# Performance work log

Measured on AMD Instinct MI355X. Metric: run time of the kernel, lower is better.

## Reference

```python
import jax, jax.numpy as jnp
import numpy as np

C = 64; NET = 32; K = 3; G = 4; GC = C // G; P = K * K
STRIDE = 1; PAD = 1; DIL = 1; OFFSET_SCALE = 1.0
BN_EPS = 1e-5; LN_EPS = 1e-6


def conv2d(x, w, b, groups=1, pad=1):
    # x: (N,C,H,W), w: (O, I//groups, kh, kw)
    y = jax.lax.conv_general_dilated(
        x, w, (1, 1), [(pad, pad), (pad, pad)],
        feature_group_count=groups,
        dimension_numbers=('NCHW', 'OIHW', 'NCHW'))
    return y + b[None, :, None, None]


def dcnv3_core(x, offset, mask):
    """Faithful port of dcnv3_core_pytorch (InternImage).
    x: (N,H,W,C) channels-last; offset: (N,H,W,G*P*2); mask: (N,H,W,G*P) (softmaxed).
    grid_sample(bilinear, zeros padding, align_corners=False) done manually."""
    xp = jnp.pad(x, ((0, 0), (PAD, PAD), (PAD, PAD), (0, 0)))
    N, Hin, Win, _ = xp.shape
    Ho, Wo = offset.shape[1], offset.shape[2]
    # reference points in normalized [0,1] coords (x first, y second)
    start = (DIL * (K - 1)) // 2 + 0.5
    ref_x = (start + jnp.arange(Wo, dtype=jnp.float32) * STRIDE) / Win  # (Wo,)
    ref_y = (start + jnp.arange(Ho, dtype=jnp.float32) * STRIDE) / Hin  # (Ho,)
    ref = jnp.stack(jnp.broadcast_arrays(ref_x[None, :], ref_y[:, None]), axis=-1)  # (Ho,Wo,2)
    # dilation grid (kernel tap offsets, torch meshgrid 'ij' flatten order: w-major)
    kv = (jnp.arange(K, dtype=jnp.float32) * DIL - (DIL * (K - 1)) // 2)
    gx, gy = jnp.meshgrid(kv / Win, kv / Hin, indexing='ij')
    grid = jnp.stack([gx, gy], -1).reshape(P, 2)  # (P,2), same for every group
    # sampling locations, normalized: (N,Ho,Wo,G,P,2)
    off = offset.reshape(N, Ho, Wo, G, P, 2) * (OFFSET_SCALE / jnp.array([Win, Hin], jnp.float32))
    loc = ref[None, :, :, None, None, :] + grid[None, None, None, None, :, :] * OFFSET_SCALE + off
    # grid_sample align_corners=False: pixel = loc*size - 0.5  (since g = 2*loc-1)
    px = loc[..., 0] * Win - 0.5
    py = loc[..., 1] * Hin - 0.5
    x0 = jnp.floor(px); y0 = jnp.floor(py)
    ix0 = x0.astype(jnp.int32); iy0 = y0.astype(jnp.int32)
    wx1 = px - x0; wy1 = py - y0; wx0 = 1.0 - wx1; wy0 = 1.0 - wy1
    xg = xp.reshape(N, Hin, Win, G, GC)
    n_idx = jnp.arange(N)[:, None, None, None, None]
    g_idx = jnp.arange(G)[None, None, None, :, None]

    def sample(ix, iy):
        valid = ((ix >= 0) & (ix < Win) & (iy >= 0) & (iy < Hin)).astype(xg.dtype)
        v = xg[n_idx, jnp.clip(iy, 0, Hin - 1), jnp.clip(ix, 0, Win - 1), g_idx]  # (N,Ho,Wo,G,P,GC)
        return v * valid[..., None]

    val = (sample(ix0, iy0) * (wx0 * wy0)[..., None]
           + sample(ix0 + 1, iy0) * (wx1 * wy0)[..., None]
           + sample(ix0, iy0 + 1) * (wx0 * wy1)[..., None]
           + sample(ix0 + 1, iy0 + 1) * (wx1 * wy1)[..., None])
    out = jnp.einsum('nhwgpc,nhwgp->nhwgc', val, mask.reshape(N, Ho, Wo, G, P))
    return out.reshape(N, Ho, Wo, C)


def setup_inputs() -> dict:
    key = jax.random.key(0)
    ks = jax.random.split(key, 16)
    N, H, W = 4, 128, 128
    f = lambda k, shp, s=1.0: jax.random.normal(k, shp, jnp.float32) * s
    return {
        'input_x': f(ks[0], (N, C, H, W)),
        'input_y': f(ks[1], (N, NET, H, W)),
        'enc_w': f(ks[2], (NET, C), 0.05), 'enc_b': jnp.zeros((NET,), jnp.float32),
        'bn_g': jnp.ones((NET,), jnp.float32), 'bn_b': jnp.zeros((NET,), jnp.float32),
        'bn_m': jnp.zeros((NET,), jnp.float32), 'bn_v': jnp.ones((NET,), jnp.float32),
        'gru_wz': f(ks[3], (NET, 2 * NET, 3, 3), 0.05), 'gru_bz': jnp.zeros((NET,), jnp.float32),
        'gru_wr': f(ks[4], (NET, 2 * NET, 3, 3), 0.05), 'gru_br': jnp.zeros((NET,), jnp.float32),
        'gru_wq': f(ks[5], (NET, 2 * NET, 3, 3), 0.05), 'gru_bq': jnp.zeros((NET,), jnp.float32),
        'dw_w': f(ks[6], (C, 1, 3, 3), 0.1), 'dw_b': jnp.zeros((C,), jnp.float32),
        'ln_g': jnp.ones((C,), jnp.float32), 'ln_b': jnp.zeros((C,), jnp.float32),
        'off_w': f(ks[7], (G * P * 2, C), 0.1), 'off_b': f(ks[8], (G * P * 2,), 0.1),
        'mask_w': f(ks[9], (G * P, C), 0.1), 'mask_b': jnp.zeros((G * P,), jnp.float32),
        'inp_w': f(ks[10], (C, C), 0.1), 'inp_b': jnp.zeros((C,), jnp.float32),
        'out_w': f(ks[11], (C, C), 0.1), 'out_b': jnp.zeros((C,), jnp.float32),
    }


def reference(input_x, input_y, enc_w, enc_b, bn_g, bn_b, bn_m, bn_v,
              gru_wz, gru_bz, gru_wr, gru_br, gru_wq, gru_bq,
              dw_w, dw_b, ln_g, ln_b, off_w, off_b, mask_w, mask_b,
              inp_w, inp_b, out_w, out_b):
    N, _, H, W = input_x.shape
    # encoder: 1x1 Conv + BN(eval) + SiLU
    e = jnp.einsum('nchw,oc->nohw', input_x, enc_w) + enc_b[None, :, None, None]
    e = (e - bn_m[None, :, None, None]) * jax.lax.rsqrt(bn_v + BN_EPS)[None, :, None, None]
    e = e * bn_g[None, :, None, None] + bn_b[None, :, None, None]
    x_en = jax.nn.silu(e)
    # ConvGRU: h' = (1-z)*h + z*q
    hx = jnp.concatenate([input_y, x_en], axis=1)
    z = jax.nn.sigmoid(conv2d(hx, gru_wz, gru_bz))
    r = jax.nn.sigmoid(conv2d(hx, gru_wr, gru_br))
    q = jnp.tanh(conv2d(jnp.concatenate([r * input_y, x_en], axis=1), gru_wq, gru_bq))
    h = (1.0 - z) * input_y + z * q  # (N,NET,H,W)
    # channels-last main path
    inp = input_x.transpose(0, 2, 3, 1)  # (N,H,W,C)
    x = inp @ inp_w.T + inp_b
    # depthwise conv on gru state -> LN (channels_last) -> GELU
    y = conv2d(h, dw_w, dw_b, groups=NET).transpose(0, 2, 3, 1)  # (N,H,W,C)
    mu = y.mean(-1, keepdims=True)
    var = ((y - mu) ** 2).mean(-1, keepdims=True)
    y = (y - mu) * jax.lax.rsqrt(var + LN_EPS) * ln_g + ln_b
    y = jax.nn.gelu(y, approximate=False)
    offset = y @ off_w.T + off_b  # (N,H,W,G*P*2)
    m = y @ mask_w.T + mask_b
    m = jax.nn.softmax(m.reshape(N, H, W, G, P), axis=-1).reshape(N, H, W, G * P)
    x = dcnv3_core(x, offset, m)
    x = x @ out_w.T + out_b
    return jax.nn.silu(x.transpose(0, 3, 1, 2)), h
```

## Files before the change

kernel.cpp:

```cpp
#include <hip/hip_runtime.h>
#include <hip/hip_bf16.h>

typedef __hip_bfloat16 bf16;
typedef short short8v __attribute__((ext_vector_type(8)));
typedef short short4v __attribute__((ext_vector_type(4)));
typedef float float4v __attribute__((ext_vector_type(4)));

static __device__ __forceinline__ float b2f(bf16 v){ return __bfloat162float(v); }
static __device__ __forceinline__ bf16 f2b(float v){ return __float2bfloat16(v); }
static __device__ __forceinline__ float bu2f(unsigned short u){ return __uint_as_float(((unsigned)u) << 16); }
static __device__ __forceinline__ short f2bs(float v){ bf16 t = __float2bfloat16(v); return *(short*)&t; }

#define WT 128
#define HWT 16384

#define OFF_ENC   0
#define OFF_ENCSC 2048
#define OFF_ENCSH 2080
#define OFF_BZ    20544
#define OFF_BR    39008
#define OFF_BQ    57472
#define OFF_DWP   57504
#define OFF_DWB   58080
#define OFF_LNG   58144
#define OFF_LNB   58208
#define OFF_OMB   65184
#define OFF_WINP  65296
#define OFF_BINP  69392
#define OFF_BOUT  73552
#define NW_TOTAL  73616
#define NBF_ZR    36864
#define NBF_Q     18432
#define NBF_OM    7168
#define NBF_OUT   4096
#define NPREP     (NW_TOTAL + NBF_ZR + NBF_Q + NBF_OM + NBF_OUT)
#define NHALO     2064
#define NTOT      (NPREP + NHALO)

#define B_WZRB  294912
#define B_WQB   368640
#define B_WOMB  405504
#define B_WOUTB 419840
#define B_HXP   428544
#define B_QINP  9081344
#define B_ZBUF  17734144
#define B_XL    428544

__global__ void k_prep(
    const float* __restrict__ enc_w, const float* __restrict__ enc_b,
    const float* __restrict__ bn_g, const float* __restrict__ bn_b,
    const float* __restrict__ bn_m, const float* __restrict__ bn_v,
    const float* __restrict__ gwz, const float* __restrict__ gbz,
    const float* __restrict__ gwr, const float* __restrict__ gbr,
    const float* __restrict__ gwq, const float* __restrict__ gbq,
    const float* __restrict__ dww, const float* __restrict__ dwb,
    const float* __restrict__ lng, const float* __restrict__ lnb,
    const float* __restrict__ offw, const float* __restrict__ offb,
    const float* __restrict__ maskw, const float* __restrict__ maskb,
    const float* __restrict__ inpw, const float* __restrict__ inpb,
    const float* __restrict__ outw, const float* __restrict__ outb,
    float* __restrict__ Wp, bf16* __restrict__ wzrb, bf16* __restrict__ wqb,
    bf16* __restrict__ womb, bf16* __restrict__ woutb,
    bf16* __restrict__ hxp, bf16* __restrict__ qinp) {
  int i = blockIdx.x * blockDim.x + threadIdx.x;
  if (i >= NTOT) return;
  if (i >= NPREP) {
    int t = i - NPREP;
    int img = t / 516, r = t % 516;
    int ph, pw;
    if (r < 130) { ph = 0; pw = r; }
    else if (r < 260) { ph = 129; pw = r - 130; }
    else if (r < 388) { ph = r - 260 + 1; pw = 0; }
    else { ph = r - 388 + 1; pw = 129; }
    size_t pb = (((size_t)img * 130 + ph) * 130 + pw) * 64;
    uint4 zz = make_uint4(0, 0, 0, 0);
    #pragma unroll
    for (int k = 0; k < 8; ++k) {
      ((uint4*)(hxp + pb))[k] = zz;
      ((uint4*)(qinp + pb))[k] = zz;
    }
    return;
  }
  if (i >= NW_TOTAL) {
    int d = i - NW_TOTAL;
    if (d < NBF_ZR) {
      int t = d / 9216, rem = d % 9216;
      int kc = rem / 512, rem2 = rem % 512;
      int ln = rem2 >> 3, j = rem2 & 7;
      int n = t * 16 + (ln & 15);
      int cin = (kc & 1) * 32 + ((ln >> 4) << 3) + j;
      int tap = kc >> 1;
      float v = (n < 32) ? gwz[(n*64 + cin)*9 + tap] : gwr[((n-32)*64 + cin)*9 + tap];
      wzrb[d] = f2b(v);
    } else if (d < NBF_ZR + NBF_Q) {
      int d2 = d - NBF_ZR;
      int t = d2 / 9216, rem = d2 % 9216;
      int kc = rem / 512, rem2 = rem % 512;
      int ln = rem2 >> 3, j = rem2 & 7;
      int n = t * 16 + (ln & 15);
      int cin = (kc & 1) * 32 + ((ln >> 4) << 3) + j;
      int tap = kc >> 1;
      wqb[d2] = f2b(gwq[(n*64 + cin)*9 + tap]);
    } else if (d < NBF_ZR + NBF_Q + NBF_OM) {
      int d3 = d - NBF_ZR - NBF_Q;
      int wv = d3 / 1024, rem = d3 % 1024;
      int kc = rem / 512, rem2 = rem % 512;
      int ln = rem2 >> 3, j = rem2 & 7;
      int jcol = wv * 16 + (ln & 15);
      int c = kc * 32 + ((ln >> 4) << 3) + j;
      float v = (jcol < 72) ? offw[jcol*64 + c] : ((jcol < 108) ? maskw[(jcol-72)*64 + c] : 0.f);
      womb[d3] = f2b(v);
    } else {
      int d4 = d - NBF_ZR - NBF_Q - NBF_OM;
      int wv = d4 / 1024, rem = d4 % 1024;
      int kc = rem / 512, rem2 = rem % 512;
      int ln = rem2 >> 3, j = rem2 & 7;
      int o = wv * 16 + (ln & 15);
      int c = kc * 32 + ((ln >> 4) << 3) + j;
      woutb[d4] = f2b(outw[o*64 + c]);
    }
    return;
  }
  float v;
  if (i < 2048) { int c = i >> 5, o = i & 31; v = enc_w[o*64 + c]; }
  else if (i < 2080) { int o = i - 2048; v = bn_g[o] * rsqrtf(bn_v[o] + 1e-5f); }
  else if (i < 2112) { int o = i - 2080;
    float sc = bn_g[o] * rsqrtf(bn_v[o] + 1e-5f);
    v = (enc_b[o] - bn_m[o]) * sc + bn_b[o]; }
  else if (i < 20544) { v = 0.f; }
  else if (i < 20576) { v = gbz[i - OFF_BZ]; }
  else if (i < 39008) { v = 0.f; }
  else if (i < 39040) { v = gbr[i - OFF_BR]; }
  else if (i < 57472) { v = 0.f; }
  else if (i < 57504) { v = gbq[i - OFF_BQ]; }
  else if (i < 58080) { int d = i - OFF_DWP; int tap = d >> 6, o = d & 63; v = dww[o*9 + tap]; }
  else if (i < 58144) { v = dwb[i - OFF_DWB]; }
  else if (i < 58208) { v = lng[i - OFF_LNG]; }
  else if (i < 58272) { v = lnb[i - OFF_LNB]; }
  else if (i < 65184) { v = 0.f; }
  else if (i < 65292) { int j = i - OFF_OMB; v = (j < 72) ? offb[j] : maskb[j-72]; }
  else if (i < 65296) { v = 0.f; }
  else if (i < 69392) { int d = i - OFF_WINP; int c = d >> 6, o = d & 63; v = inpw[o*64 + c]; }
  else if (i < 69456) { v = inpb[i - OFF_BINP]; }
  else if (i < 73552) { v = 0.f; }
  else { v = outb[i - OFF_BOUT]; }
  Wp[i] = v;
}

__global__ void __launch_bounds__(256) k_pre(
    const float* __restrict__ X, const float* __restrict__ Y,
    const float* __restrict__ Wp, bf16* __restrict__ hxp, bf16* __restrict__ qinp) {
  __shared__ float xls[4096];
  int tid = threadIdx.x;
  int px = tid & 63, sect = tid >> 6;
  int img = blockIdx.z, h = blockIdx.y, w0 = blockIdx.x * 64;
  int hw = h * WT + w0 + px;
  const float* xp = X + (size_t)img * (64 * HWT) + hw;
  #pragma unroll
  for (int i = 0; i < 16; ++i) {
    int c = sect * 16 + i;
    xls[c * 64 + px] = xp[c * HWT];
  }
  const float* yp = Y + (size_t)img * (32 * HWT) + hw;
  bf16 yv[8];
  #pragma unroll
  for (int i = 0; i < 8; ++i) yv[i] = f2b(yp[(sect * 8 + i) * HWT]);
  size_t pb = (((size_t)img * 130 + h + 1) * 130 + (w0 + px + 1)) * 64;
  *(uint4*)(hxp + pb + sect * 8) = *(const uint4*)yv;
  __syncthreads();
  float aen[8];
  #pragma unroll
  for (int o = 0; o < 8; ++o) aen[o] = 0.f;
  for (int k = 0; k < 64; ++k) {
    float a = xls[k * 64 + px];
    const float* we = Wp + OFF_ENC + k * 32 + sect * 8;
    #pragma unroll
    for (int o = 0; o < 8; ++o) aen[o] += a * we[o];
  }
  bf16 xe[8];
  #pragma unroll
  for (int o = 0; o < 8; ++o) {
    int oo = sect * 8 + o;
    float e = aen[o] * Wp[OFF_ENCSC + oo] + Wp[OFF_ENCSH + oo];
    xe[o] = f2b(e / (1.f + __expf(-e)));
  }
  *(uint4*)(hxp + pb + 32 + sect * 8) = *(const uint4*)xe;
  *(uint4*)(qinp + pb + 32 + sect * 8) = *(const uint4*)xe;
}

__global__ void __launch_bounds__(256) k_zr(
    const float* __restrict__ Wp,
    const bf16* __restrict__ hxp, const bf16* __restrict__ wzrb,
    bf16* __restrict__ qinp, bf16* __restrict__ zbuf) {
  __shared__ short zt[32 * 132];
  __shared__ short ryt[128 * 40];
  int tid = threadIdx.x;
  int wv = tid >> 6, ln = tid & 63;
  int quad = ln >> 4, lm = ln & 15;
  int img = blockIdx.z, h = blockIdx.y;
  int p0 = wv * 32;
  const short* hs = (const short*)hxp;
  const short* ws = (const short*)wzrb;
  size_t rowb = ((size_t)img * 130 + h + 1) * 130;
  const short* ab0 = hs + (rowb + p0 + lm + 1) * 64 + quad * 8;
  const short* ab1 = ab0 + 16 * 64;
  short8v a0[18], a1[18];
  #pragma unroll
  for (int kc = 0; kc < 18; ++kc) {
    const int tap = kc >> 1, cin0 = (kc & 1) * 32;
    const int dd = (tap / 3 - 1) * 130 + (tap % 3 - 1);
    a0[kc] = *(const short8v*)(ab0 + dd * 64 + cin0);
    a1[kc] = *(const short8v*)(ab1 + dd * 64 + cin0);
  }
  float4v acc[8];
  #pragma unroll
  for (int t = 0; t < 8; ++t) acc[t] = (float4v){0.f, 0.f, 0.f, 0.f};
  #pragma unroll
  for (int kc = 0; kc < 18; ++kc) {
    #pragma unroll
    for (int t = 0; t < 4; ++t) {
      short8v b = *(const short8v*)(ws + ((t * 18 + kc) * 64 + ln) * 8);
      acc[t*2]   = __builtin_amdgcn_mfma_f32_16x16x32_bf16(a0[kc], b, acc[t*2], 0, 0, 0);
      acc[t*2+1] = __builtin_amdgcn_mfma_f32_16x16x32_bf16(a1[kc], b, acc[t*2+1], 0, 0, 0);
    }
  }
  #pragma unroll
  for (int mt = 0; mt < 2; ++mt) {
    #pragma unroll
    for (int t = 0; t < 2; ++t) {
      int n = t * 16 + lm;
      float bz = Wp[OFF_BZ + n];
      short zp[4];
      #pragma unroll
      for (int ri = 0; ri < 4; ++ri)
        zp[ri] = f2bs(1.f / (1.f + __expf(-(acc[t*2+mt][ri] + bz))));
      *(short4v*)(zt + n * 132 + p0 + mt * 16 + quad * 4) = *(const short4v*)zp;
    }
  }
  #pragma unroll
  for (int mt = 0; mt < 2; ++mt) {
    #pragma unroll
    for (int t = 2; t < 4; ++t) {
      int c = (t - 2) * 16 + lm;
      float br = Wp[OFF_BR + c];
      #pragma unroll
      for (int ri = 0; ri < 4; ++ri) {
        int px = p0 + mt * 16 + quad * 4 + ri;
        float rv = 1.f / (1.f + __expf(-(acc[t*2+mt][ri] + br)));
        float yy = b2f(hxp[(rowb + px + 1) * 64 + c]);
        ryt[px * 40 + c] = f2bs(rv * yy);
      }
    }
  }
  __syncthreads();
  {
    int n2 = tid >> 3, pq = tid & 7;
    short8v z0 = *(const short8v*)(zt + n2 * 132 + pq * 16);
    short8v z1 = *(const short8v*)(zt + n2 * 132 + pq * 16 + 8);
    short* zo = (short*)zbuf + (((size_t)img * 128 + h) * 32 + n2) * 128 + pq * 16;
    *(short8v*)zo = z0;
    *(short8v*)(zo + 8) = z1;
  }
  {
    int px = tid >> 1, chalf = tid & 1;
    short8v r0 = *(const short8v*)(ryt + px * 40 + chalf * 16);
    short8v r1 = *(const short8v*)(ryt + px * 40 + chalf * 16 + 8);
    short* qo = (short*)qinp + (rowb + px + 1) * 64 + chalf * 16;
    *(short8v*)qo = r0;
    *(short8v*)(qo + 8) = r1;
  }
}

__global__ void __launch_bounds__(256) k_qg(
    const float* __restrict__ Y, const float* __restrict__ Wp,
    const bf16* __restrict__ qinp, const bf16* __restrict__ wqb,
    const bf16* __restrict__ zbuf, float* __restrict__ outh) {
  __shared__ float hout[32 * 132];
  int tid = threadIdx.x;
  int wv = tid >> 6, ln = tid & 63;
  int quad = ln >> 4, lm = ln & 15;
  int img = blockIdx.z, h = blockIdx.y;
  int p0 = wv * 32;
  const short* qs = (const short*)qinp;
  const short* ws = (const short*)wqb;
  size_t rowb = ((size_t)img * 130 + h + 1) * 130;
  const short* ab0 = qs + (rowb + p0 + lm + 1) * 64 + quad * 8;
  const short* ab1 = ab0 + 16 * 64;
  short8v a0[18], a1[18];
  #pragma unroll
  for (int kc = 0; kc < 18; ++kc) {
    const int tap = kc >> 1, cin0 = (kc & 1) * 32;
    const int dd = (tap / 3 - 1) * 130 + (tap % 3 - 1);
    a0[kc] = *(const short8v*)(ab0 + dd * 64 + cin0);
    a1[kc] = *(const short8v*)(ab1 + dd * 64 + cin0);
  }
  float4v acc[4];
  #pragma unroll
  for (int t = 0; t < 4; ++t) acc[t] = (float4v){0.f, 0.f, 0.f, 0.f};
  #pragma unroll
  for (int kc = 0; kc < 18; ++kc) {
    #pragma unroll
    for (int t = 0; t < 2; ++t) {
      short8v b = *(const short8v*)(ws + ((t * 18 + kc) * 64 + ln) * 8);
      acc[t*2]   = __builtin_amdgcn_mfma_f32_16x16x32_bf16(a0[kc], b, acc[t*2], 0, 0, 0);
      acc[t*2+1] = __builtin_amdgcn_mfma_f32_16x16x32_bf16(a1[kc], b, acc[t*2+1], 0, 0, 0);
    }
  }
  #pragma unroll
  for (int mt = 0; mt < 2; ++mt) {
    #pragma unroll
    for (int t = 0; t < 2; ++t) {
      int n = t * 16 + lm;
      float bq = Wp[OFF_BQ + n];
      float4 hv;
      hv.x = acc[t*2+mt][0] + bq; hv.y = acc[t*2+mt][1] + bq;
      hv.z = acc[t*2+mt][2] + bq; hv.w = acc[t*2+mt][3] + bq;
      *(float4*)(hout + n * 132 + p0 + mt * 16 + quad * 4) = hv;
    }
  }
  __syncthreads();
  const short* zbb = (const short*)zbuf + ((size_t)img * 128 + h) * 32 * 128;
  #pragma unroll
  for (int r = 0; r < 4; ++r) {
    int n = (tid >> 5) + r * 8;
    int px4 = (tid & 31) * 4;
    float4 hv = *(const float4*)(hout + n * 132 + px4);
    uint2 zz = *(const uint2*)(zbb + n * 128 + px4);
    size_t gb = ((size_t)img * 32 + n) * HWT + h * 128 + px4;
    float4 yv = *(const float4*)(Y + gb);
    float z0 = bu2f((unsigned short)(zz.x & 0xFFFFu)), z1 = bu2f((unsigned short)(zz.x >> 16));
    float z2 = bu2f((unsigned short)(zz.y & 0xFFFFu)), z3 = bu2f((unsigned short)(zz.y >> 16));
    float4 o;
    o.x = (1.f - z0) * yv.x + z0 * tanhf(hv.x);
    o.y = (1.f - z1) * yv.y + z1 * tanhf(hv.y);
    o.z = (1.f - z2) * yv.z + z2 * tanhf(hv.z);
    o.w = (1.f - z3) * yv.w + z3 * tanhf(hv.w);
    *(float4*)(outh + gb) = o;
  }
}

__global__ void __launch_bounds__(256) k_xl(
    const float* __restrict__ X, const float* __restrict__ Wp, bf16* __restrict__ xl) {
  __shared__ float xls[4096];
  int tid = threadIdx.x;
  int px = tid & 63, sect = tid >> 6;
  int img = blockIdx.z, h = blockIdx.y, w0 = blockIdx.x * 64;
  int hw = h * WT + w0 + px;
  const float* xp = X + (size_t)img * (64 * HWT) + hw;
  #pragma unroll
  for (int i = 0; i < 16; ++i) {
    int c = sect * 16 + i;
    xls[c * 64 + px] = xp[c * HWT];
  }
  __syncthreads();
  float acc[16];
  #pragma unroll
  for (int o = 0; o < 16; ++o) acc[o] = Wp[OFF_BINP + sect * 16 + o];
  for (int k = 0; k < 64; ++k) {
    float a = xls[k * 64 + px];
    const float* wr = Wp + OFF_WINP + k * 64 + sect * 16;
    #pragma unroll
    for (int o = 0; o < 16; ++o) acc[o] += a * wr[o];
  }
  bf16 ov[16];
  #pragma unroll
  for (int o = 0; o < 16; ++o) ov[o] = f2b(acc[o]);
  bf16* op = xl + ((size_t)img * HWT + hw) * 64 + sect * 16;
  ((uint4*)op)[0] = ((const uint4*)ov)[0];
  ((uint4*)op)[1] = ((const uint4*)ov)[1];
}

#define LDS_PSA  0
#define LDS_PSB  2048
#define LDS_STAT 4096
#define LDS_Y    4608
#define LDS_OM   13824
#define LDS_TOT  28416

__global__ void __launch_bounds__(512) k_mega(
    const float* __restrict__ Wp, const float* __restrict__ hb,
    const bf16* __restrict__ xl, const bf16* __restrict__ womb,
    const bf16* __restrict__ woutb, float* __restrict__ out0) {
  __shared__ char smem[LDS_TOT];
  float* psa  = (float*)(smem + LDS_PSA);
  float* psb  = (float*)(smem + LDS_PSB);
  float* stat = (float*)(smem + LDS_STAT);
  short* yls  = (short*)(smem + LDS_Y);
  short* omls = (short*)(smem + LDS_OM);
  short* vls  = (short*)(smem + LDS_Y);

  int tid = threadIdx.x;
  int img = blockIdx.z, h = blockIdx.y, w0 = blockIdx.x * 64;

  int wloc = tid & 63, part = tid >> 6;
  int w = w0 + wloc;
  float yv[8];
  {
    const float* hn = hb + (size_t)img * (32 * HWT);
    #pragma unroll
    for (int i = 0; i < 8; ++i) yv[i] = Wp[OFF_DWB + part*8 + i];
    #pragma unroll
    for (int tap = 0; tap < 9; ++tap) {
      int dy = tap / 3 - 1, dx = tap % 3 - 1;
      int hh = h + dy, ww = w + dx;
      bool ok = ((unsigned)hh < 128u) && ((unsigned)ww < 128u);
      int off = hh * WT + ww;
      #pragma unroll
      for (int j = 0; j < 4; ++j) {
        int cin = part * 4 + j;
        float a = ok ? hn[cin * HWT + off] : 0.f;
        yv[2*j]   += a * Wp[OFF_DWP + tap*64 + part*8 + 2*j];
        yv[2*j+1] += a * Wp[OFF_DWP + tap*64 + part*8 + 2*j+1];
      }
    }
  }
  float lsum = 0.f, lsq = 0.f;
  #pragma unroll
  for (int i = 0; i < 8; ++i) { lsum += yv[i]; lsq += yv[i]*yv[i]; }
  psa[part * 64 + wloc] = lsum;
  psb[part * 64 + wloc] = lsq;
  __syncthreads();
  if (tid < 64) {
    float s = 0.f, q = 0.f;
    #pragma unroll
    for (int p = 0; p < 8; ++p) { s += psa[p*64 + tid]; q += psb[p*64 + tid]; }
    float mu = s * (1.f/64.f);
    float var = q * (1.f/64.f) - mu * mu;
    stat[tid*2] = mu;
    stat[tid*2+1] = rsqrtf(var + 1e-6f);
  }
  __syncthreads();
  {
    float mu = stat[wloc*2], inv = stat[wloc*2+1];
    bf16 tmp[8];
    #pragma unroll
    for (int i = 0; i < 8; ++i) {
      int c = part*8 + i;
      float v = (yv[i] - mu) * inv * Wp[OFF_LNG + c] + Wp[OFF_LNB + c];
      tmp[i] = f2b(0.5f * v * (1.f + erff(v * 0.70710678118654752f)));
    }
    *(short8v*)(yls + wloc*72 + part*8) = *(const short8v*)tmp;
  }
  __syncthreads();

  int wv = tid >> 6, ln = tid & 63, quad = ln >> 4, lm = ln & 15;
  if (wv < 7) {
    const short* wb = (const short*)womb;
    float4v acc[4];
    #pragma unroll
    for (int mt = 0; mt < 4; ++mt) acc[mt] = (float4v){0.f,0.f,0.f,0.f};
    #pragma unroll
    for (int kc = 0; kc < 2; ++kc) {
      short8v b = *(const short8v*)(wb + ((wv * 2 + kc) * 64 + ln) * 8);
      #pragma unroll
      for (int mt = 0; mt < 4; ++mt) {
        short8v a = *(const short8v*)(yls + (mt*16 + lm)*72 + kc*32 + quad*8);
        acc[mt] = __builtin_amdgcn_mfma_f32_16x16x32_bf16(a, b, acc[mt], 0, 0, 0);
      }
    }
    float bias = Wp[OFF_OMB + wv*16 + lm];
    #pragma unroll
    for (int mt = 0; mt < 4; ++mt) {
      #pragma unroll
      for (int ri = 0; ri < 4; ++ri)
        omls[(mt*16 + quad*4 + ri)*114 + wv*16 + lm] = f2bs(acc[mt][ri] + bias);
    }
  }
  __syncthreads();

  {
    int px = tid >> 3, g = (tid >> 1) & 3, half = tid & 1;
    const short* oml = omls + px*114;
    float m[9];
    #pragma unroll
    for (int p = 0; p < 9; ++p) m[p] = bu2f((unsigned short)oml[72 + g*9 + p]);
    float mx = m[0];
    #pragma unroll
    for (int p = 1; p < 9; ++p) mx = fmaxf(mx, m[p]);
    float sum = 0.f;
    #pragma unroll
    for (int p = 0; p < 9; ++p) { m[p] = __expf(m[p] - mx); sum += m[p]; }
    float rs = 1.f / sum;
    int wg = w0 + px;
    const bf16* xn = xl + (size_t)img * (HWT * 64);
    float acc[8];
    #pragma unroll
    for (int i = 0; i < 8; ++i) acc[i] = 0.f;
    for (int p = 0; p < 9; ++p) {
      float bx = (float)(wg + p / 3 - 1);
      float by = (float)(h + p % 3 - 1);
      float ox = bu2f((unsigned short)oml[g*18 + p*2]);
      float oy = bu2f((unsigned short)oml[g*18 + p*2 + 1]);
      float mk = m[p] * rs;
      float pxx = bx + ox, pyy = by + oy;
      float fx = floorf(pxx), fy = floorf(pyy);
      int jx0 = (int)fx, jy0 = (int)fy;
      float wx1 = pxx - fx, wy1 = pyy - fy;
      float wx0 = 1.f - wx1, wy0 = 1.f - wy1;
      int cjx[4] = { jx0, jx0 + 1, jx0, jx0 + 1 };
      int cjy[4] = { jy0, jy0, jy0 + 1, jy0 + 1 };
      float cw[4] = { wx0*wy0, wx1*wy0, wx0*wy1, wx1*wy1 };
      #pragma unroll
      for (int k = 0; k < 4; ++k) {
        if ((unsigned)cjx[k] < 128u && (unsigned)cjy[k] < 128u) {
          float cf = mk * cw[k];
          const bf16* s = xn + (size_t)(cjy[k] * WT + cjx[k]) * 64 + g * 16 + half * 8;
          uint4 u0 = *(const uint4*)(s);
          const unsigned uu[4] = {u0.x,u0.y,u0.z,u0.w};
          #pragma unroll
          for (int q = 0; q < 4; ++q) {
            acc[2*q]     += cf * bu2f((unsigned short)(uu[q] & 0xFFFFu));
            acc[2*q + 1] += cf * bu2f((unsigned short)(uu[q] >> 16));
          }
        }
      }
    }
    bf16 tmp[8];
    #pragma unroll
    for (int i = 0; i < 8; ++i) tmp[i] = f2b(acc[i]);
    *(short8v*)(vls + px*72 + g*16 + half*8) = *(const short8v*)tmp;
  }
  __syncthreads();

  if (wv < 4) {
    const short* wb = (const short*)woutb;
    float4v acc[4];
    #pragma unroll
    for (int mt = 0; mt < 4; ++mt) acc[mt] = (float4v){0.f,0.f,0.f,0.f};
    #pragma unroll
    for (int kc = 0; kc < 2; ++kc) {
      short8v b = *(const short8v*)(wb + ((wv * 2 + kc) * 64 + ln) * 8);
      #pragma unroll
      for (int mt = 0; mt < 4; ++mt) {
        short8v a = *(const short8v*)(vls + (mt*16 + lm)*72 + kc*32 + quad*8);
        acc[mt] = __builtin_amdgcn_mfma_f32_16x16x32_bf16(a, b, acc[mt], 0, 0, 0);
      }
    }
    int ch = wv*16 + lm;
    float bias = Wp[OFF_BOUT + ch];
    #pragma unroll
    for (int mt = 0; mt < 4; ++mt) {
      float4 v;
      float s0 = acc[mt][0] + bias; v.x = s0 / (1.f + __expf(-s0));
      float s1 = acc[mt][1] + bias; v.y = s1 / (1.f + __expf(-s1));
      float s2 = acc[mt][2] + bias; v.z = s2 / (1.f + __expf(-s2));
      float s3 = acc[mt][3] + bias; v.w = s3 / (1.f + __expf(-s3));
      *(float4*)(out0 + ((size_t)img*64 + ch)*HWT + h*128 + w0 + mt*16 + quad*4) = v;
    }
  }
}

extern "C" void kernel_launch(void* const* d_in, const int* in_sizes, int n_in,
                              void* d_out, int out_size, void* d_ws, size_t ws_size,
                              hipStream_t stream) {
  const float* input_x = (const float*)d_in[0];
  const float* input_y = (const float*)d_in[1];

  float* Wp = (float*)d_ws;
  bf16* WZRB  = (bf16*)((char*)d_ws + B_WZRB);
  bf16* WQB   = (bf16*)((char*)d_ws + B_WQB);
  bf16* WOMB  = (bf16*)((char*)d_ws + B_WOMB);
  bf16* WOUTB = (bf16*)((char*)d_ws + B_WOUTB);
  bf16* HXP   = (bf16*)((char*)d_ws + B_HXP);
  bf16* QINP  = (bf16*)((char*)d_ws + B_QINP);
  bf16* ZBUF  = (bf16*)((char*)d_ws + B_ZBUF);
  bf16* XL    = (bf16*)((char*)d_ws + B_XL);
  float* out0 = (float*)d_out;
  float* outh = (float*)d_out + 4194304;

  k_prep<<<dim3((NTOT + 255)/256), dim3(256), 0, stream>>>(
      (const float*)d_in[2], (const float*)d_in[3], (const float*)d_in[4], (const float*)d_in[5],
      (const float*)d_in[6], (const float*)d_in[7], (const float*)d_in[8], (const float*)d_in[9],
      (const float*)d_in[10], (const float*)d_in[11], (const float*)d_in[12], (const float*)d_in[13],
      (const float*)d_in[14], (const float*)d_in[15], (const float*)d_in[16], (const float*)d_in[17],
      (const float*)d_in[18], (const float*)d_in[19], (const float*)d_in[20], (const float*)d_in[21],
      (const float*)d_in[22], (const float*)d_in[23], (const float*)d_in[24], (const float*)d_in[25],
      Wp, WZRB, WQB, WOMB, WOUTB, HXP, QINP);
  k_pre<<<dim3(2, 128, 4), dim3(256), 0, stream>>>(input_x, input_y, Wp, HXP, QINP);
  k_zr <<<dim3(1, 128, 4), dim3(256), 0, stream>>>(Wp, HXP, WZRB, QINP, ZBUF);
  k_qg <<<dim3(1, 128, 4), dim3(256), 0, stream>>>(input_y, Wp, QINP, WQB, ZBUF, outh);
  k_xl <<<dim3(2, 128, 4), dim3(256), 0, stream>>>(input_x, Wp, XL);
  k_mega<<<dim3(2, 128, 4), dim3(512), 0, stream>>>(Wp, outh, XL, WOMB, WOUTB, out0);
}
```

Measured before the change: 257.4 us.

## Merge weight prep with encoder stage and q-gate with input projection kernels

Folds the weight-packing kernel and the encoder/halo pre-kernel into one launch, with encoder weights and BN scale/shift staged per block in LDS instead of read from the prepped buffer. The q-gate kernel and the input-projection kernel become one launch split by block index. The q-gate A-fragments are now loaded inside the MFMA loop instead of preloaded into registers. The output projection is spread over all 8 waves with 2 tiles each instead of 4 waves doing 4 tiles, aiming to cut launch count and balance work at the cost of redundant per-block weight loads.

Result: faster. 244.2 us (-5.2%).

```diff
diff --git a/kernel.cpp b/kernel.cpp
--- a/kernel.cpp
+++ b/kernel.cpp
@@ -36,6 +36,7 @@
 #define NPREP     (NW_TOTAL + NBF_ZR + NBF_Q + NBF_OM + NBF_OUT)
 #define NHALO     2064
 #define NTOT      (NPREP + NHALO)
+#define NB_PREPB  556
 
 #define B_WZRB  294912
 #define B_WQB   368640
@@ -46,7 +47,7 @@
 #define B_ZBUF  17734144
 #define B_XL    428544
 
-__global__ void k_prep(
+__global__ void __launch_bounds__(256) k_stage1(
     const float* __restrict__ enc_w, const float* __restrict__ enc_b,
     const float* __restrict__ bn_g, const float* __restrict__ bn_b,
     const float* __restrict__ bn_m, const float* __restrict__ bn_v,
@@ -61,119 +62,130 @@
     const float* __restrict__ outw, const float* __restrict__ outb,
     float* __restrict__ Wp, bf16* __restrict__ wzrb, bf16* __restrict__ wqb,
     bf16* __restrict__ womb, bf16* __restrict__ woutb,
-    bf16* __restrict__ hxp, bf16* __restrict__ qinp) {
-  int i = blockIdx.x * blockDim.x + threadIdx.x;
-  if (i >= NTOT) return;
-  if (i >= NPREP) {
-    int t = i - NPREP;
-    int img = t / 516, r = t % 516;
-    int ph, pw;
-    if (r < 130) { ph = 0; pw = r; }
-    else if (r < 260) { ph = 129; pw = r - 130; }
-    else if (r < 388) { ph = r - 260 + 1; pw = 0; }
-    else { ph = r - 388 + 1; pw = 129; }
-    size_t pb = (((size_t)img * 130 + ph) * 130 + pw) * 64;
-    uint4 zz = make_uint4(0, 0, 0, 0);
-    #pragma unroll
-    for (int k = 0; k < 8; ++k) {
-      ((uint4*)(hxp + pb))[k] = zz;
-      ((uint4*)(qinp + pb))[k] = zz;
-    }
+    bf16* __restrict__ hxp, bf16* __restrict__ qinp,
+    const float* __restrict__ X, const float* __restrict__ Y) {
+  __shared__ float xls[4096];
+  __shared__ float ewls[2048];
+  __shared__ float escl[64];
+  int tid = threadIdx.x;
+  int b = blockIdx.x;
+
+  if (b < NB_PREPB) {
+    int i = b * 256 + tid;
+    if (i >= NTOT) return;
+    if (i >= NPREP) {
+      int t = i - NPREP;
+      int img = t / 516, r = t % 516;
+      int ph, pw;
+      if (r < 130) { ph = 0; pw = r; }
+      else if (r < 260) { ph = 129; pw = r - 130; }
+      else if (r < 388) { ph = r - 260 + 1; pw = 0; }
+      else { ph = r - 388 + 1; pw = 129; }
+      size_t pb = (((size_t)img * 130 + ph) * 130 + pw) * 64;
+      uint4 zz = make_uint4(0, 0, 0, 0);
+      #pragma unroll
+      for (int k = 0; k < 8; ++k) {
+        ((uint4*)(hxp + pb))[k] = zz;
+        ((uint4*)(qinp + pb))[k] = zz;
+      }
+      return;
+    }
+    if (i >= NW_TOTAL) {
+      int d = i - NW_TOTAL;
+      if (d < NBF_ZR) {
+        int t = d / 9216, rem = d % 9216;
+        int kc = rem / 512, rem2 = rem % 512;
+        int ln = rem2 >> 3, j = rem2 & 7;
+        int n = t * 16 + (ln & 15);
+        int cin = (kc & 1) * 32 + ((ln >> 4) << 3) + j;
+        int tap = kc >> 1;
+        float v = (n < 32) ? gwz[(n*64 + cin)*9 + tap] : gwr[((n-32)*64 + cin)*9 + tap];
+        wzrb[d] = f2b(v);
+      } else if (d < NBF_ZR + NBF_Q) {
+        int d2 = d - NBF_ZR;
+        int t = d2 / 9216, rem = d2 % 9216;
+        int kc = rem / 512, rem2 = rem % 512;
+        int ln = rem2 >> 3, j = rem2 & 7;
+        int n = t * 16 + (ln & 15);
+        int cin = (kc & 1) * 32 + ((ln >> 4) << 3) + j;
+        int tap = kc >> 1;
+        wqb[d2] = f2b(gwq[(n*64 + cin)*9 + tap]);
+      } else if (d < NBF_ZR + NBF_Q + NBF_OM) {
+        int d3 = d - NBF_ZR - NBF_Q;
+        int wv = d3 / 1024, rem = d3 % 1024;
+        int kc = rem / 512, rem2 = rem % 512;
+        int ln = rem2 >> 3, j = rem2 & 7;
+        int jcol = wv * 16 + (ln & 15);
+        int c = kc * 32 + ((ln >> 4) << 3) + j;
+        float v = (jcol < 72) ? offw[jcol*64 + c] : ((jcol < 108) ? maskw[(jcol-72)*64 + c] : 0.f);
+        womb[d3] = f2b(v);
+      } else {
+        int d4 = d - NBF_ZR - NBF_Q - NBF_OM;
+        int nt = d4 / 1024, rem = d4 % 1024;
+        int kc = rem / 512, rem2 = rem % 512;
+        int ln = rem2 >> 3, j = rem2 & 7;
+        int o = nt * 16 + (ln & 15);
+        int c = kc * 32 + ((ln >> 4) << 3) + j;
+        woutb[d4] = f2b(outw[o*64 + c]);
+      }
+      return;
+    }
+    float v;
+    if (i < 20544) { v = 0.f; }
+    else if (i < 20576) { v = gbz[i - OFF_BZ]; }
+    else if (i < 39008) { v = 0.f; }
+    else if (i < 39040) { v = gbr[i - OFF_BR]; }
+    else if (i < 57472) { v = 0.f; }
+    else if (i < 57504) { v = gbq[i - OFF_BQ]; }
+    else if (i < 58080) { int d = i - OFF_DWP; int tap = d >> 6, o = d & 63; v = dww[o*9 + tap]; }
+    else if (i < 58144) { v = dwb[i - OFF_DWB]; }
+    else if (i < 58208) { v = lng[i - OFF_LNG]; }
+    else if (i < 58272) { v = lnb[i - OFF_LNB]; }
+    else if (i < 65184) { v = 0.f; }
+    else if (i < 65292) { int j = i - OFF_OMB; v = (j < 72) ? offb[j] : maskb[j-72]; }
+    else if (i < 65296) { v = 0.f; }
+    else if (i < 69392) { int d = i - OFF_WINP; int c = d >> 6, o = d & 63; v = inpw[o*64 + c]; }
+    else if (i < 69456) { v = inpb[i - OFF_BINP]; }
+    else if (i < 73552) { v = 0.f; }
+    else { v = outb[i - OFF_BOUT]; }
+    Wp[i] = v;
     return;
   }
-  if (i >= NW_TOTAL) {
-    int d = i - NW_TOTAL;
-    if (d < NBF_ZR) {
-      int t = d / 9216, rem = d % 9216;
-      int kc = rem / 512, rem2 = rem % 512;
-      int ln = rem2 >> 3, j = rem2 & 7;
-      int n = t * 16 + (ln & 15);
-      int cin = (kc & 1) * 32 + ((ln >> 4) << 3) + j;
-      int tap = kc >> 1;
-      float v = (n < 32) ? gwz[(n*64 + cin)*9 + tap] : gwr[((n-32)*64 + cin)*9 + tap];
-      wzrb[d] = f2b(v);
-    } else if (d < NBF_ZR + NBF_Q) {
-      int d2 = d - NBF_ZR;
-      int t = d2 / 9216, rem = d2 % 9216;
-      int kc = rem / 512, rem2 = rem % 512;
-      int ln = rem2 >> 3, j = rem2 & 7;
-      int n = t * 16 + (ln & 15);
-      int cin = (kc & 1) * 32 + ((ln >> 4) << 3) + j;
-      int tap = kc >> 1;
-      wqb[d2] = f2b(gwq[(n*64 + cin)*9 + tap]);
-    } else if (d < NBF_ZR + NBF_Q + NBF_OM) {
-      int d3 = d - NBF_ZR - NBF_Q;
-      int wv = d3 / 1024, rem = d3 % 1024;
-      int kc = rem / 512, rem2 = rem % 512;
-      int ln = rem2 >> 3, j = rem2 & 7;
-      int jcol = wv * 16 + (ln & 15);
-      int c = kc * 32 + ((ln >> 4) << 3) + j;
-      float v = (jcol < 72) ? offw[jcol*64 + c] : ((jcol < 108) ? maskw[(jcol-72)*64 + c] : 0.f);
-      womb[d3] = f2b(v);
-    } else {
-      int d4 = d - NBF_ZR - NBF_Q - NBF_OM;
-      int wv = d4 / 1024, rem = d4 % 1024;
-      int kc = rem / 512, rem2 = rem % 512;
-      int ln = rem2 >> 3, j = rem2 & 7;
-      int o = wv * 16 + (ln & 15);
-      int c = kc * 32 + ((ln >> 4) << 3) + j;
-      woutb[d4] = f2b(outw[o*64 + c]);
-    }
-    return;
-  }
-  float v;
-  if (i < 2048) { int c = i >> 5, o = i & 31; v = enc_w[o*64 + c]; }
-  else if (i < 2080) { int o = i - 2048; v = bn_g[o] * rsqrtf(bn_v[o] + 1e-5f); }
-  else if (i < 2112) { int o = i - 2080;
-    float sc = bn_g[o] * rsqrtf(bn_v[o] + 1e-5f);
-    v = (enc_b[o] - bn_m[o]) * sc + bn_b[o]; }
-  else if (i < 20544) { v = 0.f; }
-  else if (i < 20576) { v = gbz[i - OFF_BZ]; }
-  else if (i < 39008) { v = 0.f; }
-  else if (i < 39040) { v = gbr[i - OFF_BR]; }
-  else if (i < 57472) { v = 0.f; }
-  else if (i < 57504) { v = gbq[i - OFF_BQ]; }
-  else if (i < 58080) { int d = i - OFF_DWP; int tap = d >> 6, o = d & 63; v = dww[o*9 + tap]; }
-  else if (i < 58144) { v = dwb[i - OFF_DWB]; }
-  else if (i < 58208) { v = lng[i - OFF_LNG]; }
-  else if (i < 58272) { v = lnb[i - OFF_LNB]; }
-  else if (i < 65184) { v = 0.f; }
-  else if (i < 65292) { int j = i - OFF_OMB; v = (j < 72) ? offb[j] : maskb[j-72]; }
-  else if (i < 65296) { v = 0.f; }
-  else if (i < 69392) { int d = i - OFF_WINP; int c = d >> 6, o = d & 63; v = inpw[o*64 + c]; }
-  else if (i < 69456) { v = inpb[i - OFF_BINP]; }
-  else if (i < 73552) { v = 0.f; }
-  else { v = outb[i - OFF_BOUT]; }
-  Wp[i] = v;
-}
-
-__global__ void __launch_bounds__(256) k_pre(
-    const float* __restrict__ X, const float* __restrict__ Y,
-    const float* __restrict__ Wp, bf16* __restrict__ hxp, bf16* __restrict__ qinp) {
-  __shared__ float xls[4096];
-  int tid = threadIdx.x;
+
+  int pb2 = b - NB_PREPB;
+  int img = pb2 >> 8, h = (pb2 >> 1) & 127, w0 = (pb2 & 1) * 64;
   int px = tid & 63, sect = tid >> 6;
-  int img = blockIdx.z, h = blockIdx.y, w0 = blockIdx.x * 64;
+  #pragma unroll
+  for (int k = 0; k < 8; ++k) {
+    int i2 = k * 256 + tid;
+    int c = i2 >> 5, o = i2 & 31;
+    ewls[i2] = enc_w[o*64 + c];
+  }
+  if (tid < 32) {
+    float sc = bn_g[tid] * rsqrtf(bn_v[tid] + 1e-5f);
+    escl[tid] = sc;
+    escl[32 + tid] = (enc_b[tid] - bn_m[tid]) * sc + bn_b[tid];
+  }
   int hw = h * WT + w0 + px;
   const float* xp = X + (size_t)img * (64 * HWT) + hw;
   #pragma unroll
-  for (int i = 0; i < 16; ++i) {
-    int c = sect * 16 + i;
+  for (int i2 = 0; i2 < 16; ++i2) {
+    int c = sect * 16 + i2;
     xls[c * 64 + px] = xp[c * HWT];
   }
   const float* yp = Y + (size_t)img * (32 * HWT) + hw;
   bf16 yv[8];
   #pragma unroll
-  for (int i = 0; i < 8; ++i) yv[i] = f2b(yp[(sect * 8 + i) * HWT]);
-  size_t pb = (((size_t)img * 130 + h + 1) * 130 + (w0 + px + 1)) * 64;
-  *(uint4*)(hxp + pb + sect * 8) = *(const uint4*)yv;
+  for (int i2 = 0; i2 < 8; ++i2) yv[i2] = f2b(yp[(sect * 8 + i2) * HWT]);
+  size_t pbb = (((size_t)img * 130 + h + 1) * 130 + (w0 + px + 1)) * 64;
+  *(uint4*)(hxp + pbb + sect * 8) = *(const uint4*)yv;
   __syncthreads();
   float aen[8];
   #pragma unroll
   for (int o = 0; o < 8; ++o) aen[o] = 0.f;
   for (int k = 0; k < 64; ++k) {
     float a = xls[k * 64 + px];
-    const float* we = Wp + OFF_ENC + k * 32 + sect * 8;
+    const float* we = ewls + k * 32 + sect * 8;
     #pragma unroll
     for (int o = 0; o < 8; ++o) aen[o] += a * we[o];
   }
@@ -181,11 +193,11 @@
   #pragma unroll
   for (int o = 0; o < 8; ++o) {
     int oo = sect * 8 + o;
-    float e = aen[o] * Wp[OFF_ENCSC + oo] + Wp[OFF_ENCSH + oo];
+    float e = aen[o] * escl[oo] + escl[32 + oo];
     xe[o] = f2b(e / (1.f + __expf(-e)));
   }
-  *(uint4*)(hxp + pb + 32 + sect * 8) = *(const uint4*)xe;
-  *(uint4*)(qinp + pb + 32 + sect * 8) = *(const uint4*)xe;
+  *(uint4*)(hxp + pbb + 32 + sect * 8) = *(const uint4*)xe;
+  *(uint4*)(qinp + pbb + 32 + sect * 8) = *(const uint4*)xe;
 }
 
 __global__ void __launch_bounds__(256) k_zr(
@@ -271,103 +283,105 @@
   }
 }
 
-__global__ void __launch_bounds__(256) k_qg(
+__global__ void __launch_bounds__(256) k_stageB(
     const float* __restrict__ Y, const float* __restrict__ Wp,
     const bf16* __restrict__ qinp, const bf16* __restrict__ wqb,
-    const bf16* __restrict__ zbuf, float* __restrict__ outh) {
-  __shared__ float hout[32 * 132];
+    const bf16* __restrict__ zbuf, float* __restrict__ outh,
+    const float* __restrict__ X, bf16* __restrict__ xl) {
+  __shared__ char sm[16896];
   int tid = threadIdx.x;
-  int wv = tid >> 6, ln = tid & 63;
-  int quad = ln >> 4, lm = ln & 15;
-  int img = blockIdx.z, h = blockIdx.y;
-  int p0 = wv * 32;
-  const short* qs = (const short*)qinp;
-  const short* ws = (const short*)wqb;
-  size_t rowb = ((size_t)img * 130 + h + 1) * 130;
-  const short* ab0 = qs + (rowb + p0 + lm + 1) * 64 + quad * 8;
-  const short* ab1 = ab0 + 16 * 64;
-  short8v a0[18], a1[18];
-  #pragma unroll
-  for (int kc = 0; kc < 18; ++kc) {
-    const int tap = kc >> 1, cin0 = (kc & 1) * 32;
-    const int dd = (tap / 3 - 1) * 130 + (tap % 3 - 1);
-    a0[kc] = *(const short8v*)(ab0 + dd * 64 + cin0);
-    a1[kc] = *(const short8v*)(ab1 + dd * 64 + cin0);
-  }
-  float4v acc[4];
-  #pragma unroll
-  for (int t = 0; t < 4; ++t) acc[t] = (float4v){0.f, 0.f, 0.f, 0.f};
-  #pragma unroll
-  for (int kc = 0; kc < 18; ++kc) {
-    #pragma unroll
-    for (int t = 0; t < 2; ++t) {
-      short8v b = *(const short8v*)(ws + ((t * 18 + kc) * 64 + ln) * 8);
-      acc[t*2]   = __builtin_amdgcn_mfma_f32_16x16x32_bf16(a0[kc], b, acc[t*2], 0, 0, 0);
-      acc[t*2+1] = __builtin_amdgcn_mfma_f32_16x16x32_bf16(a1[kc], b, acc[t*2+1], 0, 0, 0);
-    }
-  }
-  #pragma unroll
-  for (int mt = 0; mt < 2; ++mt) {
-    #pragma unroll
-    for (int t = 0; t < 2; ++t) {
-      int n = t * 16 + lm;
-      float bq = Wp[OFF_BQ + n];
-      float4 hv;
-      hv.x = acc[t*2+mt][0] + bq; hv.y = acc[t*2+mt][1] + bq;
-      hv.z = acc[t*2+mt][2] + bq; hv.w = acc[t*2+mt][3] + bq;
-      *(float4*)(hout + n * 132 + p0 + mt * 16 + quad * 4) = hv;
-    }
-  }
-  __syncthreads();
-  const short* zbb = (const short*)zbuf + ((size_t)img * 128 + h) * 32 * 128;
-  #pragma unroll
-  for (int r = 0; r < 4; ++r) {
-    int n = (tid >> 5) + r * 8;
-    int px4 = (tid & 31) * 4;
-    float4 hv = *(const float4*)(hout + n * 132 + px4);
-    uint2 zz = *(const uint2*)(zbb + n * 128 + px4);
-    size_t gb = ((size_t)img * 32 + n) * HWT + h * 128 + px4;
-    float4 yv = *(const float4*)(Y + gb);
-    float z0 = bu2f((unsigned short)(zz.x & 0xFFFFu)), z1 = bu2f((unsigned short)(zz.x >> 16));
-    float z2 = bu2f((unsigned short)(zz.y & 0xFFFFu)), z3 = bu2f((unsigned short)(zz.y >> 16));
-    float4 o;
-    o.x = (1.f - z0) * yv.x + z0 * tanhf(hv.x);
-    o.y = (1.f - z1) * yv.y + z1 * tanhf(hv.y);
-    o.z = (1.f - z2) * yv.z + z2 * tanhf(hv.z);
-    o.w = (1.f - z3) * yv.w + z3 * tanhf(hv.w);
-    *(float4*)(outh + gb) = o;
-  }
-}
-
-__global__ void __launch_bounds__(256) k_xl(
-    const float* __restrict__ X, const float* __restrict__ Wp, bf16* __restrict__ xl) {
-  __shared__ float xls[4096];
-  int tid = threadIdx.x;
-  int px = tid & 63, sect = tid >> 6;
-  int img = blockIdx.z, h = blockIdx.y, w0 = blockIdx.x * 64;
-  int hw = h * WT + w0 + px;
-  const float* xp = X + (size_t)img * (64 * HWT) + hw;
-  #pragma unroll
-  for (int i = 0; i < 16; ++i) {
-    int c = sect * 16 + i;
-    xls[c * 64 + px] = xp[c * HWT];
-  }
-  __syncthreads();
-  float acc[16];
-  #pragma unroll
-  for (int o = 0; o < 16; ++o) acc[o] = Wp[OFF_BINP + sect * 16 + o];
-  for (int k = 0; k < 64; ++k) {
-    float a = xls[k * 64 + px];
-    const float* wr = Wp + OFF_WINP + k * 64 + sect * 16;
-    #pragma unroll
-    for (int o = 0; o < 16; ++o) acc[o] += a * wr[o];
-  }
-  bf16 ov[16];
-  #pragma unroll
-  for (int o = 0; o < 16; ++o) ov[o] = f2b(acc[o]);
-  bf16* op = xl + ((size_t)img * HWT + hw) * 64 + sect * 16;
-  ((uint4*)op)[0] = ((const uint4*)ov)[0];
-  ((uint4*)op)[1] = ((const uint4*)ov)[1];
+  int b = blockIdx.x;
+
+  if (b < 512) {
+    float* hout = (float*)sm;
+    int wv = tid >> 6, ln = tid & 63;
+    int quad = ln >> 4, lm = ln & 15;
+    int img = b >> 7, h = b & 127;
+    int p0 = wv * 32;
+    const short* qs = (const short*)qinp;
+    const short* ws = (const short*)wqb;
+    size_t rowb = ((size_t)img * 130 + h + 1) * 130;
+    const short* ab0 = qs + (rowb + p0 + lm + 1) * 64 + quad * 8;
+    const short* ab1 = ab0 + 16 * 64;
+    float4v acc[4];
+    #pragma unroll
+    for (int t = 0; t < 4; ++t) acc[t] = (float4v){0.f, 0.f, 0.f, 0.f};
+    #pragma unroll
+    for (int kc = 0; kc < 18; ++kc) {
+      const int tap = kc >> 1, cin0 = (kc & 1) * 32;
+      const int dd = (tap / 3 - 1) * 130 + (tap % 3 - 1);
+      short8v a0 = *(const short8v*)(ab0 + dd * 64 + cin0);
+      short8v a1 = *(const short8v*)(ab1 + dd * 64 + cin0);
+      #pragma unroll
+      for (int t = 0; t < 2; ++t) {
+        short8v bb = *(const short8v*)(ws + ((t * 18 + kc) * 64 + ln) * 8);
+        acc[t*2]   = __builtin_amdgcn_mfma_f32_16x16x32_bf16(a0, bb, acc[t*2], 0, 0, 0);
+        acc[t*2+1] = __builtin_amdgcn_mfma_f32_16x16x32_bf16(a1, bb, acc[t*2+1], 0, 0, 0);
+      }
+    }
+    #pragma unroll
+    for (int mt = 0; mt < 2; ++mt) {
+      #pragma unroll
+      for (int t = 0; t < 2; ++t) {
+        int n = t * 16 + lm;
+        float bq = Wp[OFF_BQ + n];
+        float4 hv;
+        hv.x = acc[t*2+mt][0] + bq; hv.y = acc[t*2+mt][1] + bq;
+        hv.z = acc[t*2+mt][2] + bq; hv.w = acc[t*2+mt][3] + bq;
+        *(float4*)(hout + n * 132 + p0 + mt * 16 + quad * 4) = hv;
+      }
+    }
+    __syncthreads();
+    const short* zbb = (const short*)zbuf + ((size_t)img * 128 + h) * 32 * 128;
+    #pragma unroll
+    for (int r = 0; r < 4; ++r) {
+      int n = (tid >> 5) + r * 8;
+      int px4 = (tid & 31) * 4;
+      float4 hv = *(const float4*)(hout + n * 132 + px4);
+      uint2 zz = *(const uint2*)(zbb + n * 128 + px4);
+      size_t gb = ((size_t)img * 32 + n) * HWT + h * 128 + px4;
+      float4 yv = *(const float4*)(Y + gb);
+      float z0 = bu2f((unsigned short)(zz.x & 0xFFFFu)), z1 = bu2f((unsigned short)(zz.x >> 16));
+      float z2 = bu2f((unsigned short)(zz.y & 0xFFFFu)), z3 = bu2f((unsigned short)(zz.y >> 16));
+      float4 o;
+      o.x = (1.f - z0) * yv.x + z0 * tanhf(hv.x);
+      o.y = (1.f - z1) * yv.y + z1 * tanhf(hv.y);
+      o.z = (1.f - z2) * yv.z + z2 * tanhf(hv.z);
+      o.w = (1.f - z3) * yv.w + z3 * tanhf(hv.w);
+      *(float4*)(outh + gb) = o;
+    }
+    return;
+  }
+
+  {
+    float* xls = (float*)sm;
+    int b2 = b - 512;
+    int px = tid & 63, sect = tid >> 6;
+    int img = b2 >> 8, h = (b2 >> 1) & 127, w0 = (b2 & 1) * 64;
+    int hw = h * WT + w0 + px;
+    const float* xp = X + (size_t)img * (64 * HWT) + hw;
+    #pragma unroll
+    for (int i = 0; i < 16; ++i) {
+      int c = sect * 16 + i;
+      xls[c * 64 + px] = xp[c * HWT];
+    }
+    __syncthreads();
+    float acc[16];
+    #pragma unroll
+    for (int o = 0; o < 16; ++o) acc[o] = Wp[OFF_BINP + sect * 16 + o];
+    for (int k = 0; k < 64; ++k) {
+      float a = xls[k * 64 + px];
+      const float* wr = Wp + OFF_WINP + k * 64 + sect * 16;
+      #pragma unroll
+      for (int o = 0; o < 16; ++o) acc[o] += a * wr[o];
+    }
+    bf16 ov[16];
+    #pragma unroll
+    for (int o = 0; o < 16; ++o) ov[o] = f2b(acc[o]);
+    bf16* op = xl + ((size_t)img * HWT + hw) * 64 + sect * 16;
+    ((uint4*)op)[0] = ((const uint4*)ov)[0];
+    ((uint4*)op)[1] = ((const uint4*)ov)[1];
+  }
 }
 
 #define LDS_PSA  0
@@ -522,29 +536,26 @@
   }
   __syncthreads();
 
-  if (wv < 4) {
+  {
     const short* wb = (const short*)woutb;
-    float4v acc[4];
-    #pragma unroll
-    for (int mt = 0; mt < 4; ++mt) acc[mt] = (float4v){0.f,0.f,0.f,0.f};
-    #pragma unroll
-    for (int kc = 0; kc < 2; ++kc) {
-      short8v b = *(const short8v*)(wb + ((wv * 2 + kc) * 64 + ln) * 8);
-      #pragma unroll
-      for (int mt = 0; mt < 4; ++mt) {
+    #pragma unroll
+    for (int s = 0; s < 2; ++s) {
+      int tile = wv * 2 + s;
+      int nt = tile >> 2, mt = tile & 3;
+      float4v acc = (float4v){0.f,0.f,0.f,0.f};
+      #pragma unroll
+      for (int kc = 0; kc < 2; ++kc) {
+        short8v b = *(const short8v*)(wb + ((nt * 2 + kc) * 64 + ln) * 8);
         short8v a = *(const short8v*)(vls + (mt*16 + lm)*72 + kc*32 + quad*8);
-        acc[mt] = __builtin_amdgcn_mfma_f32_16x16x32_bf16(a, b, acc[mt], 0, 0, 0);
-      }
-    }
-    int ch = wv*16 + lm;
-    float bias = Wp[OFF_BOUT + ch];
-    #pragma unroll
-    for (int mt = 0; mt < 4; ++mt) {
+        acc = __builtin_amdgcn_mfma_f32_16x16x32_bf16(a, b, acc, 0, 0, 0);
+      }
+      int ch = nt*16 + lm;
+      float bias = Wp[OFF_BOUT + ch];
       float4 v;
-      float s0 = acc[mt][0] + bias; v.x = s0 / (1.f + __expf(-s0));
-      float s1 = acc[mt][1] + bias; v.y = s1 / (1.f + __expf(-s1));
-      float s2 = acc[mt][2] + bias; v.z = s2 / (1.f + __expf(-s2));
-      float s3 = acc[mt][3] + bias; v.w = s3 / (1.f + __expf(-s3));
+      float s0 = acc[0] + bias; v.x = s0 / (1.f + __expf(-s0));
+      float s1 = acc[1] + bias; v.y = s1 / (1.f + __expf(-s1));
+      float s2 = acc[2] + bias; v.z = s2 / (1.f + __expf(-s2));
+      float s3 = acc[3] + bias; v.w = s3 / (1.f + __expf(-s3));
       *(float4*)(out0 + ((size_t)img*64 + ch)*HWT + h*128 + w0 + mt*16 + quad*4) = v;
     }
   }
@@ -568,17 +579,15 @@
   float* out0 = (float*)d_out;
   float* outh = (float*)d_out + 4194304;
 
-  k_prep<<<dim3((NTOT + 255)/256), dim3(256), 0, stream>>>(
+  k_stage1<<<dim3(NB_PREPB + 1024), dim3(256), 0, stream>>>(
       (const float*)d_in[2], (const float*)d_in[3], (const float*)d_in[4], (const float*)d_in[5],
       (const float*)d_in[6], (const float*)d_in[7], (const float*)d_in[8], (const float*)d_in[9],
       (const float*)d_in[10], (const float*)d_in[11], (const float*)d_in[12], (const float*)d_in[13],
       (const float*)d_in[14], (const float*)d_in[15], (const float*)d_in[16], (const float*)d_in[17],
       (const float*)d_in[18], (const float*)d_in[19], (const float*)d_in[20], (const float*)d_in[21],
       (const float*)d_in[22], (const float*)d_in[23], (const float*)d_in[24], (const float*)d_in[25],
-      Wp, WZRB, WQB, WOMB, WOUTB, HXP, QINP);
-  k_pre<<<dim3(2, 128, 4), dim3(256), 0, stream>>>(input_x, input_y, Wp, HXP, QINP);
-  k_zr <<<dim3(1, 128, 4), dim3(256), 0, stream>>>(Wp, HXP, WZRB, QINP, ZBUF);
-  k_qg <<<dim3(1, 128, 4), dim3(256), 0, stream>>>(input_y, Wp, QINP, WQB, ZBUF, outh);
-  k_xl <<<dim3(2, 128, 4), dim3(256), 0, stream>>>(input_x, Wp, XL);
+      Wp, WZRB, WQB, WOMB, WOUTB, HXP, QINP, input_x, input_y);
+  k_zr<<<dim3(1, 128, 4), dim3(256), 0, stream>>>(Wp, HXP, WZRB, QINP, ZBUF);
+  k_stageB<<<dim3(1536), dim3(256), 0, stream>>>(input_y, Wp, QINP, WQB, ZBUF, outh, input_x, XL);
   k_mega<<<dim3(2, 128, 4), dim3(512), 0, stream>>>(Wp, outh, XL, WOMB, WOUTB, out0);
 }
```
